# Optimization experiments

Hardware: AMD Instinct MI355X
Metric: run time of the kernel (lower is better)

The kernel has to match this reference:

```python
import jax, jax.numpy as jnp
import numpy as np

NUM_HEADS = 16
EMBED_DIM = 2048
HEAD_DIM = EMBED_DIM // NUM_HEADS
B, S = 2, 2048


def setup_inputs() -> dict:
    key = jax.random.key(0)
    ks = jax.random.split(key, 12)
    E = EMBED_DIM
    scale = 1.0 / np.sqrt(E)  # xavier-ish for square E->E dense
    inp = {
        "x": jax.random.normal(ks[0], (B, S, E), dtype=jnp.float32),
        "sin": jax.random.uniform(ks[1], (1, NUM_HEADS, S, HEAD_DIM), dtype=jnp.float32),
        "cos": jax.random.uniform(ks[2], (1, NUM_HEADS, S, HEAD_DIM), dtype=jnp.float32),
        "mask": jax.random.randint(ks[3], (B, S, S), 0, 2, dtype=jnp.int32),
        "Wq": jax.random.normal(ks[4], (E, E), dtype=jnp.float32) * scale,
        "bq": jnp.zeros((E,), dtype=jnp.float32),
        "Wk": jax.random.normal(ks[5], (E, E), dtype=jnp.float32) * scale,
        "bk": jnp.zeros((E,), dtype=jnp.float32),
        "Wv": jax.random.normal(ks[6], (E, E), dtype=jnp.float32) * scale,
        "bv": jnp.zeros((E,), dtype=jnp.float32),
        "Wo": jax.random.normal(ks[7], (E, E), dtype=jnp.float32) * scale,
        "bo": jnp.zeros((E,), dtype=jnp.float32),
    }
    return inp


def _minus_swap_alternate(t):
    # stack([-t[...,1::2], t[...,::2]], -1).reshape(t.shape)
    return jnp.stack([-t[..., 1::2], t[..., ::2]], axis=-1).reshape(t.shape)


def _forward(x, sin, cos, mask, Wq, bq, Wk, bk, Wv, bv, Wo, bo):
    Bx, Sx, E = x.shape
    H, D = NUM_HEADS, HEAD_DIM
    q = (x @ Wq + bq).reshape(Bx, Sx, H, D).transpose(0, 2, 1, 3)  # (B,H,S,D)
    k = (x @ Wk + bk).reshape(Bx, Sx, H, D).transpose(0, 2, 1, 3)
    v = (x @ Wv + bv).reshape(Bx, Sx, H, D).transpose(0, 2, 1, 3)
    # RoPE applied post-transpose: T = q.shape[1] == H (faithful to source)
    T = q.shape[1]
    s = sin[:, :T, :, :]
    c = cos[:, :T, :, :]
    q = q * c + _minus_swap_alternate(q) * s
    k = k * c + _minus_swap_alternate(k) * s
    m = mask[:, None, :, :]  # expand_mask: (B,S,S) -> (B,1,S,S)
    logits = jnp.einsum("bhqd,bhkd->bhqk", q, k) / jnp.sqrt(jnp.float32(D))
    logits = jnp.where(m == 0, jnp.float32(-9e15), logits)
    attention = jax.nn.softmax(logits, axis=-1)          # first softmax
    values = jnp.matmul(attention, v)                    # (B,H,S,D)
    attention_weights = jax.nn.softmax(attention, axis=-1)  # redundant second softmax
    attn_output = jnp.matmul(attention_weights, values)  # (B,H,S,D)
    attn_output = attn_output.transpose(0, 2, 1, 3).reshape(Bx, Sx, E)
    out = attn_output @ Wo + bo
    return out, attention_weights


def reference(x, sin, cos, mask, Wq, bq, Wk, bk, Wv, bv, Wo, bo):
    return _forward(x, sin, cos, mask, Wq, bq, Wk, bk, Wv, bv, Wo, bo)
```

## Files before the change

kernel.cpp:

```cpp
#include <hip/hip_runtime.h>

typedef unsigned short u16;
typedef unsigned int u32;
typedef __attribute__((ext_vector_type(8))) short short8;
typedef __attribute__((ext_vector_type(4))) float floatx4;

constexpr int Bc = 2, Sc = 2048, Ec = 2048, Hc = 16, Dc = 128;
constexpr int TILE = 128, BK = 32;

__device__ __forceinline__ u16 f2bf(float f) {
  u32 u = __builtin_bit_cast(u32, f);
  u = (u + 0x7FFFu + ((u >> 16) & 1u)) >> 16;
  return (u16)u;
}

__device__ __forceinline__ float bf2f(short s) {
  u32 u = ((u32)(u16)s) << 16;
  return __builtin_bit_cast(float, u);
}

__device__ __forceinline__ short8 pack2(float4 a, float4 b) {
  short8 r;
  r[0] = (short)f2bf(a.x); r[1] = (short)f2bf(a.y);
  r[2] = (short)f2bf(a.z); r[3] = (short)f2bf(a.w);
  r[4] = (short)f2bf(b.x); r[5] = (short)f2bf(b.y);
  r[6] = (short)f2bf(b.z); r[7] = (short)f2bf(b.w);
  return r;
}

__device__ __forceinline__ void glds16(const u16* g, u16* l) {
  __builtin_amdgcn_global_load_lds(
      (const __attribute__((address_space(1))) u32*)g,
      (__attribute__((address_space(3))) u32*)l, 16, 0, 0);
}

__device__ __forceinline__ void gemm_core(const u16* __restrict__ A, int lda,
                                          const u16* __restrict__ Bt, int ldb,
                                          int K, int m0, int n0,
                                          u16* smA, u16* smB,
                                          floatx4 (*acc)[4]) {
  const int t = threadIdx.x;
  const int lane = t & 63;
  const int w = t >> 6;
  const int wr = (w >> 1) * 64, wc = (w & 1) * 64;
  const int l15 = lane & 15, q = lane >> 4;

  const int r0 = t >> 2;
  const int c0 = (t & 3) ^ (r0 & 3);
  const u16* A0 = A + (size_t)(m0 + r0) * lda + c0 * 8;
  const u16* A1 = A0 + (size_t)64 * lda;
  const u16* B0 = Bt + (size_t)(n0 + r0) * ldb + c0 * 8;
  const u16* B1 = B0 + (size_t)64 * ldb;
  u16* dA0 = smA + w * 512;
  u16* dA1 = smA + 2048 + w * 512;
  u16* dB0 = smB + w * 512;
  u16* dB1 = smB + 2048 + w * 512;

  for (int k0 = 0; k0 < K; k0 += BK) {
    glds16(A0 + k0, dA0);
    glds16(A1 + k0, dA1);
    glds16(B0 + k0, dB0);
    glds16(B1 + k0, dB1);
    __syncthreads();

    short8 af[4], bfr[4];
    #pragma unroll
    for (int i = 0; i < 4; i++) {
      int ra = wr + i * 16 + l15;
      af[i] = *(const short8*)&smA[ra * BK + ((q ^ (ra & 3)) << 3)];
      int rb = wc + i * 16 + l15;
      bfr[i] = *(const short8*)&smB[rb * BK + ((q ^ (rb & 3)) << 3)];
    }
    #pragma unroll
    for (int mi = 0; mi < 4; mi++)
      #pragma unroll
      for (int ni = 0; ni < 4; ni++)
        acc[mi][ni] = __builtin_amdgcn_mfma_f32_16x16x32_bf16(af[mi], bfr[ni], acc[mi][ni], 0, 0, 0);
    __syncthreads();
  }
}

__global__ __launch_bounds__(256) void transpose_w(
    const float* __restrict__ Wq, const float* __restrict__ Wk,
    const float* __restrict__ Wv, const float* __restrict__ Wo,
    u16* __restrict__ WT, u16* __restrict__ WoT) {
  __shared__ float tile[32][33];
  const int z = blockIdx.z;
  const float* W = (z == 0) ? Wq : (z == 1) ? Wk : (z == 2) ? Wv : Wo;
  u16* dst = (z < 3) ? (WT + (size_t)z * Ec * Ec) : WoT;
  const int n0 = blockIdx.x * 32, k0 = blockIdx.y * 32;
  const int tx = threadIdx.x, ty = threadIdx.y;
  #pragma unroll
  for (int i = 0; i < 4; i++)
    tile[ty + 8 * i][tx] = W[(size_t)(k0 + ty + 8 * i) * Ec + n0 + tx];
  __syncthreads();
  #pragma unroll
  for (int i = 0; i < 4; i++)
    dst[(size_t)(n0 + ty + 8 * i) * Ec + k0 + tx] = f2bf(tile[tx][ty + 8 * i]);
}

__global__ __launch_bounds__(256) void xcvt_kernel(const float* __restrict__ x,
                                                   u16* __restrict__ xb,
                                                   float* __restrict__ s1) {
  const int i = blockIdx.x * 256 + threadIdx.x;
  const float4 f0 = ((const float4*)x)[(size_t)i * 2];
  const float4 f1 = ((const float4*)x)[(size_t)i * 2 + 1];
  *(short8*)&xb[(size_t)i * 8] = pack2(f0, f1);
  if (blockIdx.x < 64)
    ((float4*)s1)[i] = make_float4(0.f, 0.f, 0.f, 0.f);
}

__global__ __launch_bounds__(256) void qkv_kernel(
    const u16* __restrict__ xb, const u16* __restrict__ WT,
    const float* __restrict__ bq, const float* __restrict__ bk, const float* __restrict__ bv,
    const float* __restrict__ sinp, const float* __restrict__ cosp,
    u16* __restrict__ qr, u16* __restrict__ kr, u16* __restrict__ vT) {
  __shared__ __align__(16) u16 smA[TILE * BK];
  __shared__ __align__(16) u16 smB[TILE * BK];
  floatx4 acc[4][4] = {};
  const int m0 = blockIdx.y * TILE, n0 = blockIdx.x * TILE;
  gemm_core(xb, Ec, WT, Ec, Ec, m0, n0, smA, smB, acc);

  const int t = threadIdx.x, lane = t & 63, w = t >> 6;
  const int wr = (w >> 1) * 64, wc = (w & 1) * 64, l15 = lane & 15, q = lane >> 4;
  #pragma unroll
  for (int mi = 0; mi < 4; mi++) {
    #pragma unroll
    for (int ni = 0; ni < 4; ni++) {
      const int gcol = n0 + wc + ni * 16 + l15;
      const int which = gcol >> 11;
      const int e = gcol & 2047, h = e >> 7, d = e & 127;
      const float* bp = (which == 0) ? bq : (which == 1) ? bk : bv;
      const float bias = bp[e];
      #pragma unroll
      for (int rr = 0; rr < 4; rr++) {
        const int grow = m0 + wr + mi * 16 + q * 4 + rr;
        const int b = grow >> 11, s = grow & 2047;
        float val = acc[mi][ni][rr] + bias;
        float pv = __shfl_xor(val, 1);
        if (which < 2) {
          const size_t sc = ((size_t)h * Sc + s) * Dc + d;
          const float c = cosp[sc], sn = sinp[sc];
          const float o = val * c + ((d & 1) ? pv : -pv) * sn;
          u16* dst = which ? kr : qr;
          dst[(((size_t)b * Hc + h) * Sc + s) * Dc + d] = f2bf(o);
        } else {
          vT[(((size_t)b * Hc + h) * Dc + d) * Sc + s] = f2bf(val);
        }
      }
    }
  }
}

__global__ __launch_bounds__(256) void logits_kernel(
    const u16* __restrict__ qr, const u16* __restrict__ kr,
    const int* __restrict__ maskp, u16* __restrict__ Pbuf, float* __restrict__ s1) {
  __shared__ __align__(16) u16 smA[TILE * BK];
  __shared__ __align__(16) u16 smB[TILE * BK];
  floatx4 acc[4][4] = {};
  const int z = blockIdx.z;
  const int m0 = blockIdx.y * TILE, n0 = blockIdx.x * TILE;
  gemm_core(qr + (size_t)z * Sc * Dc, Dc, kr + (size_t)z * Sc * Dc, Dc, Dc, m0, n0, smA, smB, acc);

  u16* Pp = Pbuf + (size_t)z * Sc * Sc;
  const int b = z >> 4;
  const float scale = 0.08838834764831845f;
  const int t = threadIdx.x, lane = t & 63, w = t >> 6;
  const int wr = (w >> 1) * 64, wc = (w & 1) * 64, l15 = lane & 15, q = lane >> 4;
  float rs[4][4];
  #pragma unroll
  for (int mi = 0; mi < 4; mi++)
    #pragma unroll
    for (int rr = 0; rr < 4; rr++) rs[mi][rr] = 0.f;

  #pragma unroll
  for (int mi = 0; mi < 4; mi++)
    #pragma unroll
    for (int ni = 0; ni < 4; ni++) {
      const int gcol = n0 + wc + ni * 16 + l15;
      #pragma unroll
      for (int rr = 0; rr < 4; rr++) {
        const int grow = m0 + wr + mi * 16 + q * 4 + rr;
        const int mv = maskp[((size_t)b * Sc + grow) * Sc + gcol];
        const float val = mv ? acc[mi][ni][rr] * scale : -9.0e15f;
        const float pe = __expf(val);
        rs[mi][rr] += pe;
        Pp[(size_t)grow * Sc + gcol] = f2bf(pe);
      }
    }
  #pragma unroll
  for (int mi = 0; mi < 4; mi++)
    #pragma unroll
    for (int rr = 0; rr < 4; rr++) {
      float xs = rs[mi][rr];
      xs += __shfl_xor(xs, 1);
      xs += __shfl_xor(xs, 2);
      xs += __shfl_xor(xs, 4);
      xs += __shfl_xor(xs, 8);
      if (l15 == 0)
        atomicAdd(&s1[z * Sc + m0 + wr + mi * 16 + q * 4 + rr], xs);
    }
}

__global__ __launch_bounds__(256) void av_kernel(
    const u16* __restrict__ P, const u16* __restrict__ vT,
    const float* __restrict__ s1, u16* __restrict__ valT, float* __restrict__ s2) {
  __shared__ __align__(16) u16 smA[TILE * BK];
  __shared__ __align__(16) u16 smB[TILE * BK];
  floatx4 acc[4][4] = {};
  const int z = blockIdx.z;
  const int m0 = blockIdx.y * TILE;
  const int t = threadIdx.x, lane = t & 63, w = t >> 6;
  const int wr = (w >> 1) * 64, wc = (w & 1) * 64;
  const int l15 = lane & 15, q = lane >> 4;

  const int r0 = t >> 2;
  const int c0 = (t & 3) ^ (r0 & 3);
  const u16* Pb = P + (size_t)z * Sc * Sc;
  const u16* A0 = Pb + (size_t)(m0 + r0) * Sc + c0 * 8;
  const u16* A1 = A0 + (size_t)64 * Sc;
  const u16* Bb = vT + (size_t)z * Dc * Sc;
  const u16* B0 = Bb + (size_t)r0 * Sc + c0 * 8;
  const u16* B1 = B0 + (size_t)64 * Sc;
  u16* dA0 = smA + w * 512;
  u16* dA1 = smA + 2048 + w * 512;
  u16* dB0 = smB + w * 512;
  u16* dB1 = smB + 2048 + w * 512;

  const float inv1a = 1.0f / s1[z * Sc + m0 + r0];
  const float inv1b = 1.0f / s1[z * Sc + m0 + r0 + 64];
  float s2a = 0.0f, s2b = 0.0f;

  for (int k0 = 0; k0 < Sc; k0 += BK) {
    glds16(A0 + k0, dA0);
    glds16(A1 + k0, dA1);
    glds16(B0 + k0, dB0);
    glds16(B1 + k0, dB1);
    __syncthreads();

    short8 af[4], bfr[4];
    #pragma unroll
    for (int i = 0; i < 4; i++) {
      int ra = wr + i * 16 + l15;
      af[i] = *(const short8*)&smA[ra * BK + ((q ^ (ra & 3)) << 3)];
      int rb = wc + i * 16 + l15;
      bfr[i] = *(const short8*)&smB[rb * BK + ((q ^ (rb & 3)) << 3)];
    }
    short8 pa = *(const short8*)&smA[t * 8];
    short8 pb = *(const short8*)&smA[2048 + t * 8];

    #pragma unroll
    for (int mi = 0; mi < 4; mi++)
      #pragma unroll
      for (int ni = 0; ni < 4; ni++)
        acc[mi][ni] = __builtin_amdgcn_mfma_f32_16x16x32_bf16(af[mi], bfr[ni], acc[mi][ni], 0, 0, 0);

    #pragma unroll
    for (int j = 0; j < 8; j++) {
      s2a += __expf(bf2f(pa[j]) * inv1a);
      s2b += __expf(bf2f(pb[j]) * inv1b);
    }
    __syncthreads();
  }

  s2a += __shfl_xor(s2a, 1); s2a += __shfl_xor(s2a, 2);
  s2b += __shfl_xor(s2b, 1); s2b += __shfl_xor(s2b, 2);
  if ((t & 3) == 0) {
    s2[z * Sc + m0 + r0] = s2a;
    s2[z * Sc + m0 + r0 + 64] = s2b;
  }

  float iv[4][4];
  #pragma unroll
  for (int mi = 0; mi < 4; mi++)
    #pragma unroll
    for (int rr = 0; rr < 4; rr++)
      iv[mi][rr] = 1.0f / s1[z * Sc + m0 + wr + mi * 16 + q * 4 + rr];

  u16* C = valT + (size_t)z * Dc * Sc;
  #pragma unroll
  for (int mi = 0; mi < 4; mi++)
    #pragma unroll
    for (int ni = 0; ni < 4; ni++) {
      const int gcol = wc + ni * 16 + l15;
      #pragma unroll
      for (int rr = 0; rr < 4; rr++) {
        const int grow = m0 + wr + mi * 16 + q * 4 + rr;
        C[(size_t)gcol * Sc + grow] = f2bf(acc[mi][ni][rr] * iv[mi][rr]);
      }
    }
}

__global__ __launch_bounds__(256) void wv_kernel(
    const u16* __restrict__ P, const u16* __restrict__ valT,
    const float* __restrict__ s1, const float* __restrict__ s2,
    float* __restrict__ a2out, u16* __restrict__ aox) {
  __shared__ __align__(16) u16 smA[TILE * BK];
  __shared__ __align__(16) u16 smB[TILE * BK];
  floatx4 acc[4][4] = {};
  const int z = blockIdx.z;
  const int m0 = blockIdx.y * TILE;
  const int t = threadIdx.x;
  const int r = t >> 1, cg = (t & 1) * 2, sw = r & 3;
  const int lane = t & 63, w = t >> 6;
  const int wr = (w >> 1) * 64, wc = (w & 1) * 64;
  const int l15 = lane & 15, q = lane >> 4;

  const int r0 = t >> 2;
  const int c0 = (t & 3) ^ (r0 & 3);
  const u16* Bb = valT + (size_t)z * Dc * Sc;
  const u16* B0 = Bb + (size_t)r0 * Sc + c0 * 8;
  const u16* B1 = B0 + (size_t)64 * Sc;
  u16* dB0 = smB + w * 512;
  u16* dB1 = smB + 2048 + w * 512;

  const u16* Prow = P + (size_t)z * Sc * Sc + (size_t)(m0 + r) * Sc + cg * 8;
  float* Orow = a2out + (size_t)z * Sc * Sc + (size_t)(m0 + r) * Sc + cg * 8;
  const float inv1 = 1.0f / s1[z * Sc + m0 + r];
  const float inv2 = 1.0f / s2[z * Sc + m0 + r];

  for (int k0 = 0; k0 < Sc; k0 += BK) {
    glds16(B0 + k0, dB0);
    glds16(B1 + k0, dB1);

    short8 p0 = *(const short8*)(Prow + k0);
    short8 p1 = *(const short8*)(Prow + k0 + 8);
    float4 f[4];
    float* e = (float*)f;
    #pragma unroll
    for (int j = 0; j < 8; j++) e[j] = __expf(bf2f(p0[j]) * inv1) * inv2;
    #pragma unroll
    for (int j = 0; j < 8; j++) e[8 + j] = __expf(bf2f(p1[j]) * inv1) * inv2;
    #pragma unroll
    for (int j = 0; j < 4; j++) ((float4*)(Orow + k0))[j] = f[j];
    short8 a0 = pack2(f[0], f[1]);
    short8 a1v = pack2(f[2], f[3]);
    *(short8*)&smA[r * BK + (((cg + 0) ^ sw) << 3)] = a0;
    *(short8*)&smA[r * BK + (((cg + 1) ^ sw) << 3)] = a1v;
    __syncthreads();

    short8 af[4], bfr[4];
    #pragma unroll
    for (int i = 0; i < 4; i++) {
      int ra = wr + i * 16 + l15;
      af[i] = *(const short8*)&smA[ra * BK + ((q ^ (ra & 3)) << 3)];
      int rb = wc + i * 16 + l15;
      bfr[i] = *(const short8*)&smB[rb * BK + ((q ^ (rb & 3)) << 3)];
    }
    #pragma unroll
    for (int mi = 0; mi < 4; mi++)
      #pragma unroll
      for (int ni = 0; ni < 4; ni++)
        acc[mi][ni] = __builtin_amdgcn_mfma_f32_16x16x32_bf16(af[mi], bfr[ni], acc[mi][ni], 0, 0, 0);
    __syncthreads();
  }

  const int b = z >> 4, h = z & 15;
  #pragma unroll
  for (int mi = 0; mi < 4; mi++)
    #pragma unroll
    for (int ni = 0; ni < 4; ni++) {
      const int gcol = wc + ni * 16 + l15;
      #pragma unroll
      for (int rr = 0; rr < 4; rr++) {
        const int grow = m0 + wr + mi * 16 + q * 4 + rr;
        aox[((size_t)b * Sc + grow) * Ec + h * Dc + gcol] = f2bf(acc[mi][ni][rr]);
      }
    }
}

__global__ __launch_bounds__(256) void out_kernel(
    const u16* __restrict__ aox, const u16* __restrict__ WoT,
    const float* __restrict__ bo, float* __restrict__ outp) {
  __shared__ __align__(16) u16 smA[TILE * BK];
  __shared__ __align__(16) u16 smB[TILE * BK];
  floatx4 acc[4][4] = {};
  const int m0 = blockIdx.y * TILE, n0 = blockIdx.x * TILE;
  gemm_core(aox, Ec, WoT, Ec, Ec, m0, n0, smA, smB, acc);

  const int t = threadIdx.x, lane = t & 63, w = t >> 6;
  const int wr = (w >> 1) * 64, wc = (w & 1) * 64, l15 = lane & 15, q = lane >> 4;
  #pragma unroll
  for (int mi = 0; mi < 4; mi++)
    #pragma unroll
    for (int ni = 0; ni < 4; ni++) {
      const int gcol = n0 + wc + ni * 16 + l15;
      const float bias = bo[gcol];
      #pragma unroll
      for (int rr = 0; rr < 4; rr++) {
        const int grow = m0 + wr + mi * 16 + q * 4 + rr;
        outp[(size_t)grow * Ec + gcol] = acc[mi][ni][rr] + bias;
      }
    }
}

extern "C" void kernel_launch(void* const* d_in, const int* in_sizes, int n_in,
                              void* d_out, int out_size, void* d_ws, size_t ws_size,
                              hipStream_t stream) {
  const float* x     = (const float*)d_in[0];
  const float* sinp  = (const float*)d_in[1];
  const float* cosp  = (const float*)d_in[2];
  const int*   maskp = (const int*)d_in[3];
  const float* Wq    = (const float*)d_in[4];
  const float* bq    = (const float*)d_in[5];
  const float* Wk    = (const float*)d_in[6];
  const float* bk    = (const float*)d_in[7];
  const float* Wv    = (const float*)d_in[8];
  const float* bv    = (const float*)d_in[9];
  const float* Wo    = (const float*)d_in[10];
  const float* bo    = (const float*)d_in[11];

  float* out0  = (float*)d_out;
  float* attnL = out0 + (size_t)Bc * Sc * Ec;

  u16* wsp  = (u16*)d_ws;
  u16* WT   = wsp;
  u16* WoT  = WT + (size_t)3 * Ec * Ec;
  u16* xb   = WoT + (size_t)Ec * Ec;
  u16* qr   = xb + (size_t)Bc * Sc * Ec;
  u16* kr   = qr + (size_t)Bc * Hc * Sc * Dc;
  u16* vT   = kr + (size_t)Bc * Hc * Sc * Dc;
  u16* valT = vT + (size_t)Bc * Hc * Sc * Dc;
  u16* aox  = valT + (size_t)Bc * Hc * Sc * Dc;
  float* s1 = (float*)(aox + (size_t)Bc * Sc * Ec);
  float* s2 = s1 + (size_t)Bc * Hc * Sc;
  u16* Pbuf = (u16*)(s2 + (size_t)Bc * Hc * Sc);

  transpose_w<<<dim3(64, 64, 4), dim3(32, 8), 0, stream>>>(Wq, Wk, Wv, Wo, WT, WoT);
  xcvt_kernel<<<dim3(4096), 256, 0, stream>>>(x, xb, s1);
  qkv_kernel<<<dim3(48, 32), 256, 0, stream>>>(xb, WT, bq, bk, bv, sinp, cosp, qr, kr, vT);
  logits_kernel<<<dim3(16, 16, 32), 256, 0, stream>>>(qr, kr, maskp, Pbuf, s1);
  av_kernel<<<dim3(1, 16, 32), 256, 0, stream>>>(Pbuf, vT, s1, valT, s2);
  wv_kernel<<<dim3(1, 16, 32), 256, 0, stream>>>(Pbuf, valT, s1, s2, attnL, aox);
  out_kernel<<<dim3(16, 32), 256, 0, stream>>>(aox, WoT, bo, out0);
}
```

Before: 1.304 ms.

## Double-buffer GEMM shared-memory tiles and bit-pack the attention mask

Converts all GEMM main loops (the shared gemm_core, av_kernel and wv_kernel) to double-buffered LDS staging. The next K-slice is prefetched into the alternate buffer while MFMAs run on the current one, so each iteration needs one barrier instead of two. Adds a mask-packing kernel that compresses the int32 mask into one bit per element, so logits_kernel reads 32x less mask data; it is re-run every call. Doubled LDS per block may reduce occupancy, and the wv_kernel prefetch now also overlaps its exp/softmax staging work.

After: 1.354 ms. 1.04x slower.

```diff
diff --git a/kernel.cpp b/kernel.cpp
--- a/kernel.cpp
+++ b/kernel.cpp
@@ -7,6 +7,7 @@
 
 constexpr int Bc = 2, Sc = 2048, Ec = 2048, Hc = 16, Dc = 128;
 constexpr int TILE = 128, BK = 32;
+constexpr int BUF = TILE * BK;
 
 __device__ __forceinline__ u16 f2bf(float f) {
   u32 u = __builtin_bit_cast(u32, f);
@@ -56,20 +57,28 @@
   u16* dB0 = smB + w * 512;
   u16* dB1 = smB + 2048 + w * 512;
 
-  for (int k0 = 0; k0 < K; k0 += BK) {
-    glds16(A0 + k0, dA0);
-    glds16(A1 + k0, dA1);
-    glds16(B0 + k0, dB0);
-    glds16(B1 + k0, dB1);
-    __syncthreads();
-
+  glds16(A0, dA0); glds16(A1, dA1);
+  glds16(B0, dB0); glds16(B1, dB1);
+  __syncthreads();
+
+  const int ns = K / BK;
+  int cur = 0;
+  for (int s = 0; s < ns; s++) {
+    if (s + 1 < ns) {
+      const int k1 = (s + 1) * BK;
+      const int off = (cur ^ 1) * BUF;
+      glds16(A0 + k1, dA0 + off); glds16(A1 + k1, dA1 + off);
+      glds16(B0 + k1, dB0 + off); glds16(B1 + k1, dB1 + off);
+    }
+    const u16* sA = smA + cur * BUF;
+    const u16* sB = smB + cur * BUF;
     short8 af[4], bfr[4];
     #pragma unroll
     for (int i = 0; i < 4; i++) {
       int ra = wr + i * 16 + l15;
-      af[i] = *(const short8*)&smA[ra * BK + ((q ^ (ra & 3)) << 3)];
+      af[i] = *(const short8*)&sA[ra * BK + ((q ^ (ra & 3)) << 3)];
       int rb = wc + i * 16 + l15;
-      bfr[i] = *(const short8*)&smB[rb * BK + ((q ^ (rb & 3)) << 3)];
+      bfr[i] = *(const short8*)&sB[rb * BK + ((q ^ (rb & 3)) << 3)];
     }
     #pragma unroll
     for (int mi = 0; mi < 4; mi++)
@@ -77,6 +86,7 @@
       for (int ni = 0; ni < 4; ni++)
         acc[mi][ni] = __builtin_amdgcn_mfma_f32_16x16x32_bf16(af[mi], bfr[ni], acc[mi][ni], 0, 0, 0);
     __syncthreads();
+    cur ^= 1;
   }
 }
 
@@ -110,13 +120,29 @@
     ((float4*)s1)[i] = make_float4(0.f, 0.f, 0.f, 0.f);
 }
 
+__global__ __launch_bounds__(256) void maskpack_kernel(const int* __restrict__ mp,
+                                                       u32* __restrict__ mb) {
+  const int i = blockIdx.x * 256 + threadIdx.x;
+  const int4* src = (const int4*)mp + (size_t)i * 8;
+  u32 wv = 0;
+  #pragma unroll
+  for (int j = 0; j < 8; j++) {
+    const int4 v = src[j];
+    wv |= (u32)(v.x != 0) << (j * 4 + 0);
+    wv |= (u32)(v.y != 0) << (j * 4 + 1);
+    wv |= (u32)(v.z != 0) << (j * 4 + 2);
+    wv |= (u32)(v.w != 0) << (j * 4 + 3);
+  }
+  mb[i] = wv;
+}
+
 __global__ __launch_bounds__(256) void qkv_kernel(
     const u16* __restrict__ xb, const u16* __restrict__ WT,
     const float* __restrict__ bq, const float* __restrict__ bk, const float* __restrict__ bv,
     const float* __restrict__ sinp, const float* __restrict__ cosp,
     u16* __restrict__ qr, u16* __restrict__ kr, u16* __restrict__ vT) {
-  __shared__ __align__(16) u16 smA[TILE * BK];
-  __shared__ __align__(16) u16 smB[TILE * BK];
+  __shared__ __align__(16) u16 smA[2 * BUF];
+  __shared__ __align__(16) u16 smB[2 * BUF];
   floatx4 acc[4][4] = {};
   const int m0 = blockIdx.y * TILE, n0 = blockIdx.x * TILE;
   gemm_core(xb, Ec, WT, Ec, Ec, m0, n0, smA, smB, acc);
@@ -154,9 +180,9 @@
 
 __global__ __launch_bounds__(256) void logits_kernel(
     const u16* __restrict__ qr, const u16* __restrict__ kr,
-    const int* __restrict__ maskp, u16* __restrict__ Pbuf, float* __restrict__ s1) {
-  __shared__ __align__(16) u16 smA[TILE * BK];
-  __shared__ __align__(16) u16 smB[TILE * BK];
+    const u32* __restrict__ mb, u16* __restrict__ Pbuf, float* __restrict__ s1) {
+  __shared__ __align__(16) u16 smA[2 * BUF];
+  __shared__ __align__(16) u16 smB[2 * BUF];
   floatx4 acc[4][4] = {};
   const int z = blockIdx.z;
   const int m0 = blockIdx.y * TILE, n0 = blockIdx.x * TILE;
@@ -167,46 +193,39 @@
   const float scale = 0.08838834764831845f;
   const int t = threadIdx.x, lane = t & 63, w = t >> 6;
   const int wr = (w >> 1) * 64, wc = (w & 1) * 64, l15 = lane & 15, q = lane >> 4;
-  float rs[4][4];
+  const int wbase = (n0 + wc) >> 5;
+
   #pragma unroll
   for (int mi = 0; mi < 4; mi++)
     #pragma unroll
-    for (int rr = 0; rr < 4; rr++) rs[mi][rr] = 0.f;
-
-  #pragma unroll
-  for (int mi = 0; mi < 4; mi++)
-    #pragma unroll
-    for (int ni = 0; ni < 4; ni++) {
-      const int gcol = n0 + wc + ni * 16 + l15;
-      #pragma unroll
-      for (int rr = 0; rr < 4; rr++) {
-        const int grow = m0 + wr + mi * 16 + q * 4 + rr;
-        const int mv = maskp[((size_t)b * Sc + grow) * Sc + gcol];
+    for (int rr = 0; rr < 4; rr++) {
+      const int grow = m0 + wr + mi * 16 + q * 4 + rr;
+      const u32* mrow = mb + ((size_t)b * Sc + grow) * (Sc / 32) + wbase;
+      const u32 w0 = mrow[0], w1 = mrow[1];
+      float rsv = 0.f;
+      #pragma unroll
+      for (int ni = 0; ni < 4; ni++) {
+        const int gcol = n0 + wc + ni * 16 + l15;
+        const u32 mw = (ni < 2) ? w0 : w1;
+        const int mv = (mw >> (gcol & 31)) & 1;
         const float val = mv ? acc[mi][ni][rr] * scale : -9.0e15f;
         const float pe = __expf(val);
-        rs[mi][rr] += pe;
+        rsv += pe;
         Pp[(size_t)grow * Sc + gcol] = f2bf(pe);
       }
-    }
-  #pragma unroll
-  for (int mi = 0; mi < 4; mi++)
-    #pragma unroll
-    for (int rr = 0; rr < 4; rr++) {
-      float xs = rs[mi][rr];
-      xs += __shfl_xor(xs, 1);
-      xs += __shfl_xor(xs, 2);
-      xs += __shfl_xor(xs, 4);
-      xs += __shfl_xor(xs, 8);
-      if (l15 == 0)
-        atomicAdd(&s1[z * Sc + m0 + wr + mi * 16 + q * 4 + rr], xs);
+      rsv += __shfl_xor(rsv, 1);
+      rsv += __shfl_xor(rsv, 2);
+      rsv += __shfl_xor(rsv, 4);
+      rsv += __shfl_xor(rsv, 8);
+      if (l15 == 0) atomicAdd(&s1[z * Sc + grow], rsv);
     }
 }
 
 __global__ __launch_bounds__(256) void av_kernel(
     const u16* __restrict__ P, const u16* __restrict__ vT,
     const float* __restrict__ s1, u16* __restrict__ valT, float* __restrict__ s2) {
-  __shared__ __align__(16) u16 smA[TILE * BK];
-  __shared__ __align__(16) u16 smB[TILE * BK];
+  __shared__ __align__(16) u16 smA[2 * BUF];
+  __shared__ __align__(16) u16 smB[2 * BUF];
   floatx4 acc[4][4] = {};
   const int z = blockIdx.z;
   const int m0 = blockIdx.y * TILE;
@@ -231,23 +250,31 @@
   const float inv1b = 1.0f / s1[z * Sc + m0 + r0 + 64];
   float s2a = 0.0f, s2b = 0.0f;
 
-  for (int k0 = 0; k0 < Sc; k0 += BK) {
-    glds16(A0 + k0, dA0);
-    glds16(A1 + k0, dA1);
-    glds16(B0 + k0, dB0);
-    glds16(B1 + k0, dB1);
-    __syncthreads();
-
+  glds16(A0, dA0); glds16(A1, dA1);
+  glds16(B0, dB0); glds16(B1, dB1);
+  __syncthreads();
+
+  const int ns = Sc / BK;
+  int cur = 0;
+  for (int s = 0; s < ns; s++) {
+    if (s + 1 < ns) {
+      const int k1 = (s + 1) * BK;
+      const int off = (cur ^ 1) * BUF;
+      glds16(A0 + k1, dA0 + off); glds16(A1 + k1, dA1 + off);
+      glds16(B0 + k1, dB0 + off); glds16(B1 + k1, dB1 + off);
+    }
+    const u16* sA = smA + cur * BUF;
+    const u16* sB = smB + cur * BUF;
     short8 af[4], bfr[4];
     #pragma unroll
     for (int i = 0; i < 4; i++) {
       int ra = wr + i * 16 + l15;
-      af[i] = *(const short8*)&smA[ra * BK + ((q ^ (ra & 3)) << 3)];
+      af[i] = *(const short8*)&sA[ra * BK + ((q ^ (ra & 3)) << 3)];
       int rb = wc + i * 16 + l15;
-      bfr[i] = *(const short8*)&smB[rb * BK + ((q ^ (rb & 3)) << 3)];
-    }
-    short8 pa = *(const short8*)&smA[t * 8];
-    short8 pb = *(const short8*)&smA[2048 + t * 8];
+      bfr[i] = *(const short8*)&sB[rb * BK + ((q ^ (rb & 3)) << 3)];
+    }
+    short8 pa = *(const short8*)&sA[t * 8];
+    short8 pb = *(const short8*)&sA[2048 + t * 8];
 
     #pragma unroll
     for (int mi = 0; mi < 4; mi++)
@@ -261,6 +288,7 @@
       s2b += __expf(bf2f(pb[j]) * inv1b);
     }
     __syncthreads();
+    cur ^= 1;
   }
 
   s2a += __shfl_xor(s2a, 1); s2a += __shfl_xor(s2a, 2);
@@ -295,8 +323,8 @@
     const u16* __restrict__ P, const u16* __restrict__ valT,
     const float* __restrict__ s1, const float* __restrict__ s2,
     float* __restrict__ a2out, u16* __restrict__ aox) {
-  __shared__ __align__(16) u16 smA[TILE * BK];
-  __shared__ __align__(16) u16 smB[TILE * BK];
+  __shared__ __align__(16) u16 smA[2 * BUF];
+  __shared__ __align__(16) u16 smB[2 * BUF];
   floatx4 acc[4][4] = {};
   const int z = blockIdx.z;
   const int m0 = blockIdx.y * TILE;
@@ -319,10 +347,7 @@
   const float inv1 = 1.0f / s1[z * Sc + m0 + r];
   const float inv2 = 1.0f / s2[z * Sc + m0 + r];
 
-  for (int k0 = 0; k0 < Sc; k0 += BK) {
-    glds16(B0 + k0, dB0);
-    glds16(B1 + k0, dB1);
-
+  auto stageA = [&](int k0, int off) {
     short8 p0 = *(const short8*)(Prow + k0);
     short8 p1 = *(const short8*)(Prow + k0 + 8);
     float4 f[4];
@@ -335,17 +360,32 @@
     for (int j = 0; j < 4; j++) ((float4*)(Orow + k0))[j] = f[j];
     short8 a0 = pack2(f[0], f[1]);
     short8 a1v = pack2(f[2], f[3]);
-    *(short8*)&smA[r * BK + (((cg + 0) ^ sw) << 3)] = a0;
-    *(short8*)&smA[r * BK + (((cg + 1) ^ sw) << 3)] = a1v;
-    __syncthreads();
-
+    *(short8*)&smA[off + r * BK + (((cg + 0) ^ sw) << 3)] = a0;
+    *(short8*)&smA[off + r * BK + (((cg + 1) ^ sw) << 3)] = a1v;
+  };
+
+  glds16(B0, dB0); glds16(B1, dB1);
+  stageA(0, 0);
+  __syncthreads();
+
+  const int ns = Sc / BK;
+  int cur = 0;
+  for (int s = 0; s < ns; s++) {
+    if (s + 1 < ns) {
+      const int k1 = (s + 1) * BK;
+      const int off = (cur ^ 1) * BUF;
+      glds16(B0 + k1, dB0 + off); glds16(B1 + k1, dB1 + off);
+      stageA(k1, off);
+    }
+    const u16* sA = smA + cur * BUF;
+    const u16* sB = smB + cur * BUF;
     short8 af[4], bfr[4];
     #pragma unroll
     for (int i = 0; i < 4; i++) {
       int ra = wr + i * 16 + l15;
-      af[i] = *(const short8*)&smA[ra * BK + ((q ^ (ra & 3)) << 3)];
+      af[i] = *(const short8*)&sA[ra * BK + ((q ^ (ra & 3)) << 3)];
       int rb = wc + i * 16 + l15;
-      bfr[i] = *(const short8*)&smB[rb * BK + ((q ^ (rb & 3)) << 3)];
+      bfr[i] = *(const short8*)&sB[rb * BK + ((q ^ (rb & 3)) << 3)];
     }
     #pragma unroll
     for (int mi = 0; mi < 4; mi++)
@@ -353,6 +393,7 @@
       for (int ni = 0; ni < 4; ni++)
         acc[mi][ni] = __builtin_amdgcn_mfma_f32_16x16x32_bf16(af[mi], bfr[ni], acc[mi][ni], 0, 0, 0);
     __syncthreads();
+    cur ^= 1;
   }
 
   const int b = z >> 4, h = z & 15;
@@ -372,8 +413,8 @@
 __global__ __launch_bounds__(256) void out_kernel(
     const u16* __restrict__ aox, const u16* __restrict__ WoT,
     const float* __restrict__ bo, float* __restrict__ outp) {
-  __shared__ __align__(16) u16 smA[TILE * BK];
-  __shared__ __align__(16) u16 smB[TILE * BK];
+  __shared__ __align__(16) u16 smA[2 * BUF];
+  __shared__ __align__(16) u16 smB[2 * BUF];
   floatx4 acc[4][4] = {};
   const int m0 = blockIdx.y * TILE, n0 = blockIdx.x * TILE;
   gemm_core(aox, Ec, WoT, Ec, Ec, m0, n0, smA, smB, acc);
@@ -425,11 +466,13 @@
   float* s1 = (float*)(aox + (size_t)Bc * Sc * Ec);
   float* s2 = s1 + (size_t)Bc * Hc * Sc;
   u16* Pbuf = (u16*)(s2 + (size_t)Bc * Hc * Sc);
+  u32* mb   = (u32*)(Pbuf + (size_t)Bc * Hc * Sc * Sc);
 
   transpose_w<<<dim3(64, 64, 4), dim3(32, 8), 0, stream>>>(Wq, Wk, Wv, Wo, WT, WoT);
   xcvt_kernel<<<dim3(4096), 256, 0, stream>>>(x, xb, s1);
+  maskpack_kernel<<<dim3(1024), 256, 0, stream>>>(maskp, mb);
   qkv_kernel<<<dim3(48, 32), 256, 0, stream>>>(xb, WT, bq, bk, bv, sinp, cosp, qr, kr, vT);
-  logits_kernel<<<dim3(16, 16, 32), 256, 0, stream>>>(qr, kr, maskp, Pbuf, s1);
+  logits_kernel<<<dim3(16, 16, 32), 256, 0, stream>>>(qr, kr, mb, Pbuf, s1);
   av_kernel<<<dim3(1, 16, 32), 256, 0, stream>>>(Pbuf, vT, s1, valT, s2);
   wv_kernel<<<dim3(1, 16, 32), 256, 0, stream>>>(Pbuf, valT, s1, s2, attnL, aox);
   out_kernel<<<dim3(16, 32), 256, 0, stream>>>(aox, WoT, bo, out0);
```
